# Kernel tuning notes

Measured on AMD Instinct MI355X. Metric: run time of the kernel, lower is better.

Reference implementation:

```python
import jax, jax.numpy as jnp
import numpy as np

NUM_HEADS = 8

def setup_inputs() -> dict:
    key = jax.random.key(0)
    ks = jax.random.split(key, 6)
    B, nW, F_W, ED = 8, 64, 128, 512
    x = jax.random.normal(ks[0], (B * nW, F_W, ED), dtype=jnp.float32)
    adj_mask = jax.random.normal(ks[1], (B, NUM_HEADS, F_W, F_W), dtype=jnp.float32)
    qkv_w = jax.random.normal(ks[2], (ED, 3 * ED), dtype=jnp.float32) * (ED ** -0.5)
    qkv_b = jax.random.normal(ks[3], (3 * ED,), dtype=jnp.float32) * 0.02
    proj_w = jax.random.normal(ks[4], (ED, ED), dtype=jnp.float32) * (ED ** -0.5)
    proj_b = jax.random.normal(ks[5], (ED,), dtype=jnp.float32) * 0.02
    return {"x": x, "adj_mask": adj_mask, "qkv_w": qkv_w, "qkv_b": qkv_b,
            "proj_w": proj_w, "proj_b": proj_b, "B": B, "nW": nW}

def reference(x, adj_mask, qkv_w, qkv_b, proj_w, proj_b, B, nW):
    B_nW, F_W, ED = x.shape
    H = NUM_HEADS
    hd = ED // H
    scale = hd ** -0.5
    # qkv projection: [B_nW, F_W, 3, H, hd]
    qkv = (x @ qkv_w + qkv_b).reshape(B_nW, F_W, 3, H, hd)
    qkv = jnp.transpose(qkv, (2, 0, 3, 1, 4))  # [3, B_nW, H, F_W, hd]
    q, k, v = qkv[0], qkv[1], qkv[2]
    attn = jnp.einsum('bhqd,bhkd->bhqk', q * scale, k)  # [B_nW, H, F_W, F_W]
    # additive adjacency mask, broadcast over windows
    attn = attn.reshape(B, nW, H, F_W, F_W) + adj_mask[:, None]
    attn = attn.reshape(B_nW, H, F_W, F_W)
    attn = jax.nn.softmax(attn, axis=-1)
    out = jnp.einsum('bhqk,bhkd->bhqd', attn, v)  # [B_nW, H, F_W, hd]
    out = jnp.transpose(out, (0, 2, 1, 3)).reshape(B_nW, F_W, ED)
    return out @ proj_w + proj_b
```

## Files before the change

### kernel.cpp

```cpp
#include <hip/hip_runtime.h>

typedef __bf16 bf16_t;
typedef __bf16 bf16x8 __attribute__((ext_vector_type(8)));
typedef float f32x4 __attribute__((ext_vector_type(4)));

#define MFMA16(a, b, c) __builtin_amdgcn_mfma_f32_16x16x32_bf16(a, b, c, 0, 0, 0)

#define F_W 128
#define ED 512
#define NH 8
#define HD 64
#define NTOK 65536

typedef const __attribute__((address_space(1))) void gvoid_t;
typedef __attribute__((address_space(3))) void lvoid_t;
__device__ __forceinline__ void gload16(const void* g, void* l) {
    __builtin_amdgcn_global_load_lds((gvoid_t*)g, (lvoid_t*)l, 16, 0, 0);
}

__device__ __forceinline__ int swz32(int row) { return ((row >> 1) & 3) << 3; }

__global__ __launch_bounds__(256) void prep_kernel(
    const float* __restrict__ qkv_w,
    const float* __restrict__ proj_w,
    bf16_t* __restrict__ qkv_wt,
    bf16_t* __restrict__ proj_wt) {
    int idx = blockIdx.x * 256 + threadIdx.x;
    if (idx < 1536 * 512) {
        int n = idx >> 9, k = idx & 511;
        qkv_wt[idx] = (bf16_t)qkv_w[k * 1536 + n];
    }
    if (idx < 512 * 512) {
        int n = idx >> 9, k = idx & 511;
        proj_wt[idx] = (bf16_t)proj_w[k * 512 + n];
    }
}

__global__ __launch_bounds__(256) void prep_x_kernel(
    const float* __restrict__ x, bf16_t* __restrict__ xbf) {
    size_t i = ((size_t)blockIdx.x * 256 + threadIdx.x) * 8;
    float4 v0 = *(const float4*)(x + i);
    float4 v1 = *(const float4*)(x + i + 4);
    bf16x8 o = {(bf16_t)v0.x, (bf16_t)v0.y, (bf16_t)v0.z, (bf16_t)v0.w,
                (bf16_t)v1.x, (bf16_t)v1.y, (bf16_t)v1.z, (bf16_t)v1.w};
    *(bf16x8*)(xbf + i) = o;
}

__global__ __launch_bounds__(256, 2) void qkv_gemm_kernel(
    const bf16_t* __restrict__ xbf,
    const bf16_t* __restrict__ qkv_wt,
    const float* __restrict__ qkv_b,
    bf16_t* qk_ws,
    bf16_t* vt_ws) {
    __shared__ __align__(16) char sm[49152];
    bf16_t* tb = (bf16_t*)sm;

    const int tid = threadIdx.x;
    const int wave = tid >> 6, lane = tid & 63;
    const int lrow = lane & 15, lgrp = lane >> 4;
    const int wm = wave >> 1, wn = wave & 1;
    const int bid = blockIdx.x;
    const int idx = bid >> 3;
    const int mt_l = idx / 6;
    const int nt = idx - mt_l * 6;
    const int mtile = (bid & 7) * 64 + mt_l;
    const size_t m0 = (size_t)mtile * 128;
    const int n0 = nt * 256;

    const int row16 = lane >> 2;
    const int scol = ((lane & 3) * 8) ^ swz32(row16);

    f32x4 acc[4][8];
#pragma unroll
    for (int mf = 0; mf < 4; ++mf)
#pragma unroll
        for (int nf = 0; nf < 8; ++nf) acc[mf][nf] = (f32x4)0.0f;

    for (int kc = 0; kc < 8; ++kc) {
        const int k0 = kc * 64;
        __syncthreads();
#pragma unroll
        for (int s = 0; s < 2; ++s) {
            bf16_t* As = (bf16_t*)(sm + s * 8192);
            bf16_t* Bs = (bf16_t*)(sm + 16384 + s * 16384);
#pragma unroll
            for (int i = 0; i < 2; ++i) {
                int c = wave * 2 + i;
                gload16(xbf + (m0 + c * 16 + row16) * 512 + k0 + s * 32 + scol,
                        As + c * 512);
            }
#pragma unroll
            for (int i = 0; i < 4; ++i) {
                int c = wave * 4 + i;
                gload16(qkv_wt + (size_t)(n0 + c * 16 + row16) * 512 + k0 + s * 32 + scol,
                        Bs + c * 512);
            }
        }
        __syncthreads();

#pragma unroll
        for (int kb = 0; kb < 2; ++kb) {
            bf16_t* As = (bf16_t*)(sm + kb * 8192);
            bf16_t* Bs = (bf16_t*)(sm + 16384 + kb * 16384);
            bf16x8 a[4], b[8];
#pragma unroll
            for (int mf = 0; mf < 4; ++mf) {
                int row = wm * 64 + mf * 16 + lrow;
                a[mf] = *(const bf16x8*)(As + row * 32 + ((lgrp * 8) ^ swz32(row)));
            }
#pragma unroll
            for (int nf = 0; nf < 8; ++nf) {
                int rw = wn * 128 + nf * 16 + lrow;
                b[nf] = *(const bf16x8*)(Bs + rw * 32 + ((lgrp * 8) ^ swz32(rw)));
            }
#pragma unroll
            for (int mf = 0; mf < 4; ++mf)
#pragma unroll
                for (int nf = 0; nf < 8; ++nf)
                    acc[mf][nf] = MFMA16(a[mf], b[nf], acc[mf][nf]);
        }
    }

    if (nt < 4) {
        const float scale = (nt < 2) ? 0.125f : 1.0f;
#pragma unroll
        for (int nf = 0; nf < 8; ++nf) {
            int col = n0 + wn * 128 + nf * 16 + lrow;
            float bv = qkv_b[col];
#pragma unroll
            for (int mf = 0; mf < 4; ++mf)
#pragma unroll
                for (int j = 0; j < 4; ++j) {
                    int r = wm * 64 + mf * 16 + lgrp * 4 + j;
                    qk_ws[(m0 + r) * 1024 + col] =
                        (bf16_t)((acc[mf][nf][j] + bv) * scale);
                }
        }
    } else {
#pragma unroll
        for (int hh = 0; hh < 4; ++hh) {
            int h = (nt - 4) * 4 + hh;
            __syncthreads();
            if (wn == (hh >> 1)) {
#pragma unroll
                for (int nfl = 0; nfl < 4; ++nfl) {
                    int nf = (hh & 1) * 4 + nfl;
                    int d = nfl * 16 + lrow;
                    float bv = qkv_b[1024 + (nt - 4) * 256 + hh * 64 + d];
#pragma unroll
                    for (int mf = 0; mf < 4; ++mf)
#pragma unroll
                        for (int j = 0; j < 4; ++j) {
                            int r = wm * 64 + mf * 16 + lgrp * 4 + j;
                            tb[r * 72 + d] = (bf16_t)(acc[mf][nf][j] + bv);
                        }
                }
            }
            __syncthreads();
            {
                int d = tid & 63;
                int kh = tid >> 6;
                bf16_t* outp = vt_ws + ((size_t)(mtile * 8 + h) * 64 + d) * 128 + kh * 32;
#pragma unroll
                for (int o = 0; o < 4; ++o) {
                    bf16x8 v;
#pragma unroll
                    for (int e = 0; e < 8; ++e)
                        v[e] = tb[(kh * 32 + o * 8 + e) * 72 + d];
                    *(bf16x8*)(outp + o * 8) = v;
                }
            }
        }
    }
}

__global__ __launch_bounds__(512, 4) void attn_kernel(
    bf16_t* qk_ws,
    const bf16_t* __restrict__ vt_ws,
    const float* __restrict__ adj) {
    __shared__ __align__(16) char sm[32768];
    bf16_t* k_lds  = (bf16_t*)sm;
    bf16_t* vt_lds = (bf16_t*)(sm + 16384);
    bf16_t* pbuf   = (bf16_t*)sm;

    const int tid = threadIdx.x;
    const int wave = tid >> 6, lane = tid & 63;
    const int lrow = lane & 15, lgrp = lane >> 4;
    const int bid = blockIdx.x;
    const int w = (bid & 7) * 64 + (bid >> 6);
    const int h = (bid >> 3) & 7;
    const int bidx = bid & 7;

    bf16_t* qrow = qk_ws + (size_t)w * 128 * 1024;

    {
        const int krow_l = lane >> 3;
        const int kcol_l = ((lane & 7) * 8) ^ ((krow_l & 7) << 3);
#pragma unroll
        for (int i = 0; i < 2; ++i) {
            int c = wave * 2 + i;
            gload16(qrow + (size_t)(c * 8 + krow_l) * 1024 + 512 + h * 64 + kcol_l,
                    k_lds + c * 512);
        }
    }
    {
        const bf16_t* vtb = vt_ws + (size_t)(w * 8 + h) * 64 * 128;
        const int vrow_l = lane >> 4;
#pragma unroll
        for (int i = 0; i < 2; ++i) {
            int c = wave * 2 + i;
            int d = c * 4 + vrow_l;
            int vcol = ((lane & 15) * 8) ^ ((d & 7) << 3);
            gload16(vtb + (size_t)d * 128 + vcol, vt_lds + c * 512);
        }
    }
    bf16x8 aq[2];
    {
        int row = wave * 16 + lrow;
#pragma unroll
        for (int kb = 0; kb < 2; ++kb)
            aq[kb] = *(const bf16x8*)(qrow + (size_t)row * 1024 + h * 64 + kb * 32 + lgrp * 8);
    }
    __syncthreads();

    f32x4 sacc[8];
#pragma unroll
    for (int nf = 0; nf < 8; ++nf) sacc[nf] = (f32x4)0.0f;
#pragma unroll
    for (int kb = 0; kb < 2; ++kb) {
        bf16x8 b[8];
#pragma unroll
        for (int nf = 0; nf < 8; ++nf) {
            int row = nf * 16 + lrow;
            b[nf] = *(const bf16x8*)(k_lds + row * 64 + ((kb * 32 + lgrp * 8) ^ ((row & 7) << 3)));
        }
#pragma unroll
        for (int nf = 0; nf < 8; ++nf)
            sacc[nf] = MFMA16(aq[kb], b[nf], sacc[nf]);
    }

    const float* mbase = adj + ((size_t)(bidx * NH + h)) * F_W * F_W;
#pragma unroll
    for (int j = 0; j < 4; ++j) {
        int row = wave * 16 + lgrp * 4 + j;
        const float* mrow = mbase + (size_t)row * F_W;
        float mx = -1e30f;
#pragma unroll
        for (int nf = 0; nf < 8; ++nf) {
            sacc[nf][j] += mrow[nf * 16 + lrow];
            mx = fmaxf(mx, sacc[nf][j]);
        }
#pragma unroll
        for (int d = 1; d < 16; d <<= 1) mx = fmaxf(mx, __shfl_xor(mx, d));
        float sum = 0.f;
#pragma unroll
        for (int nf = 0; nf < 8; ++nf) {
            float p = exp2f((sacc[nf][j] - mx) * 1.44269504f);
            sacc[nf][j] = p;
            sum += p;
        }
#pragma unroll
        for (int d = 1; d < 16; d <<= 1) sum += __shfl_xor(sum, d);
        float r = 1.0f / sum;
#pragma unroll
        for (int nf = 0; nf < 8; ++nf) sacc[nf][j] *= r;
    }
    __syncthreads();

    f32x4 oacc[4];
#pragma unroll
    for (int nf = 0; nf < 4; ++nf) oacc[nf] = (f32x4)0.0f;

#pragma unroll
    for (int kb = 0; kb < 4; ++kb) {
#pragma unroll
        for (int nn = 0; nn < 2; ++nn) {
            int nf = kb * 2 + nn;
            int kk = nn * 16 + lrow;
#pragma unroll
            for (int j = 0; j < 4; ++j) {
                int r = wave * 16 + lgrp * 4 + j;
                pbuf[r * 40 + kk] = (bf16_t)(sacc[nf][j]);
            }
        }
        __syncthreads();
        bf16x8 a = *(const bf16x8*)(pbuf + (wave * 16 + lrow) * 40 + lgrp * 8);
        bf16x8 b[4];
#pragma unroll
        for (int nf = 0; nf < 4; ++nf) {
            int d = nf * 16 + lrow;
            b[nf] = *(const bf16x8*)(vt_lds + d * 128 + ((kb * 32 + lgrp * 8) ^ ((d & 7) << 3)));
        }
#pragma unroll
        for (int nf = 0; nf < 4; ++nf)
            oacc[nf] = MFMA16(a, b[nf], oacc[nf]);
        __syncthreads();
    }

#pragma unroll
    for (int nf = 0; nf < 4; ++nf) {
        int ocol = h * 64 + nf * 16 + lrow;
#pragma unroll
        for (int j = 0; j < 4; ++j) {
            int r = wave * 16 + lgrp * 4 + j;
            qrow[(size_t)r * 1024 + ocol] = (bf16_t)oacc[nf][j];
        }
    }
}

__global__ __launch_bounds__(256, 2) void proj_kernel(
    const bf16_t* __restrict__ a_g,
    const bf16_t* __restrict__ bt_g,
    const float* __restrict__ bias,
    float* __restrict__ out) {
    __shared__ __align__(16) char sm_[49152];
    const int tid = threadIdx.x;
    const int wave = tid >> 6, lane = tid & 63;
    const int lrow = lane & 15, lgrp = lane >> 4;
    const int wm = wave >> 1, wn = wave & 1;
    const int bid = blockIdx.x;
    const int idx = bid >> 3;
    const int mtile = (bid & 7) * 64 + (idx >> 1);
    const int ntile = idx & 1;
    const size_t m0 = (size_t)mtile * 128;
    const int n0 = ntile * 256;
    const int row16 = lane >> 2;
    const int scol = ((lane & 3) * 8) ^ swz32(row16);

    f32x4 acc[4][8];
#pragma unroll
    for (int mf = 0; mf < 4; ++mf)
#pragma unroll
        for (int nf = 0; nf < 8; ++nf) acc[mf][nf] = (f32x4)0.0f;

    for (int kc = 0; kc < 8; ++kc) {
        const int k0 = kc * 64;
        __syncthreads();
#pragma unroll
        for (int s = 0; s < 2; ++s) {
            bf16_t* As = (bf16_t*)(sm_ + s * 8192);
            bf16_t* Bs = (bf16_t*)(sm_ + 16384 + s * 16384);
#pragma unroll
            for (int i = 0; i < 2; ++i) {
                int c = wave * 2 + i;
                gload16(a_g + (m0 + c * 16 + row16) * 1024 + k0 + s * 32 + scol,
                        As + c * 512);
            }
#pragma unroll
            for (int i = 0; i < 4; ++i) {
                int c = wave * 4 + i;
                gload16(bt_g + (size_t)(n0 + c * 16 + row16) * 512 + k0 + s * 32 + scol,
                        Bs + c * 512);
            }
        }
        __syncthreads();

#pragma unroll
        for (int kb = 0; kb < 2; ++kb) {
            bf16_t* As = (bf16_t*)(sm_ + kb * 8192);
            bf16_t* Bs = (bf16_t*)(sm_ + 16384 + kb * 16384);
            bf16x8 a[4], b[8];
#pragma unroll
            for (int mf = 0; mf < 4; ++mf) {
                int row = wm * 64 + mf * 16 + lrow;
                a[mf] = *(const bf16x8*)(As + row * 32 + ((lgrp * 8) ^ swz32(row)));
            }
#pragma unroll
            for (int nf = 0; nf < 8; ++nf) {
                int rw = wn * 128 + nf * 16 + lrow;
                b[nf] = *(const bf16x8*)(Bs + rw * 32 + ((lgrp * 8) ^ swz32(rw)));
            }
#pragma unroll
            for (int mf = 0; mf < 4; ++mf)
#pragma unroll
                for (int nf = 0; nf < 8; ++nf)
                    acc[mf][nf] = MFMA16(a[mf], b[nf], acc[mf][nf]);
        }
    }

#pragma unroll
    for (int nf = 0; nf < 8; ++nf) {
        int col = n0 + wn * 128 + nf * 16 + lrow;
        float bv = bias[col];
#pragma unroll
        for (int mf = 0; mf < 4; ++mf)
#pragma unroll
            for (int j = 0; j < 4; ++j) {
                size_t row = m0 + wm * 64 + mf * 16 + lgrp * 4 + j;
                out[row * 512 + col] = acc[mf][nf][j] + bv;
            }
    }
}

extern "C" void kernel_launch(void* const* d_in, const int* in_sizes, int n_in,
                              void* d_out, int out_size, void* d_ws, size_t ws_size,
                              hipStream_t stream) {
    const float* x      = (const float*)d_in[0];
    const float* adj    = (const float*)d_in[1];
    const float* qkv_w  = (const float*)d_in[2];
    const float* qkv_b  = (const float*)d_in[3];
    const float* proj_w = (const float*)d_in[4];
    const float* proj_b = (const float*)d_in[5];
    float* out = (float*)d_out;

    bf16_t* qk_ws   = (bf16_t*)d_ws;
    bf16_t* vt_ws   = qk_ws + (size_t)NTOK * 1024;
    bf16_t* qkv_wt  = vt_ws + (size_t)4096 * 64 * 128;
    bf16_t* proj_wt = qkv_wt + 1536 * 512;
    bf16_t* xbf = (bf16_t*)d_out;

    prep_kernel<<<3072, 256, 0, stream>>>(qkv_w, proj_w, qkv_wt, proj_wt);
    prep_x_kernel<<<NTOK * ED / 8 / 256, 256, 0, stream>>>(x, xbf);
    qkv_gemm_kernel<<<3072, 256, 0, stream>>>(xbf, qkv_wt, qkv_b, qk_ws, vt_ws);
    attn_kernel<<<4096, 512, 0, stream>>>(qk_ws, vt_ws, adj);
    proj_kernel<<<1024, 256, 0, stream>>>(qk_ws, proj_wt, proj_b, out);
}
```

Before: 299.8 us.

## Enlarge QKV GEMM tile to 256x256 with a 4-stage LDS pipeline

The QKV projection GEMM now runs 512 threads per block on a 256x256 output tile instead of 256 threads on a 128x256 tile. It keeps a four-deep ring of LDS buffers (128KB) filled by direct global-to-LDS loads, using explicit vmcnt waits, barriers and raised scheduling priority around the MFMA blocks. The aim is to overlap global loads with matrix math and to reuse each loaded operand across more output. The V-transpose epilogue is adjusted so one tile covers two windows. The large LDS footprint limits each CU to one block, and the hand-tuned wait counts are fragile.

```diff
diff --git a/kernel.cpp b/kernel.cpp
--- a/kernel.cpp
+++ b/kernel.cpp
@@ -46,92 +46,140 @@
     *(bf16x8*)(xbf + i) = o;
 }
 
-__global__ __launch_bounds__(256, 2) void qkv_gemm_kernel(
+__global__ __launch_bounds__(512, 2) void qkv_gemm_kernel(
     const bf16_t* __restrict__ xbf,
     const bf16_t* __restrict__ qkv_wt,
     const float* __restrict__ qkv_b,
     bf16_t* qk_ws,
     bf16_t* vt_ws) {
-    __shared__ __align__(16) char sm[49152];
-    bf16_t* tb = (bf16_t*)sm;
+    __shared__ __align__(16) char smem[131072];
+    bf16_t* tb = (bf16_t*)smem;
 
     const int tid = threadIdx.x;
     const int wave = tid >> 6, lane = tid & 63;
     const int lrow = lane & 15, lgrp = lane >> 4;
-    const int wm = wave >> 1, wn = wave & 1;
+    const int wm = wave >> 2;
+    const int wn = wave & 3;
     const int bid = blockIdx.x;
     const int idx = bid >> 3;
     const int mt_l = idx / 6;
     const int nt = idx - mt_l * 6;
-    const int mtile = (bid & 7) * 64 + mt_l;
-    const size_t m0 = (size_t)mtile * 128;
+    const int mtile = (bid & 7) * 32 + mt_l;
+    const size_t m0 = (size_t)mtile * 256;
     const int n0 = nt * 256;
 
     const int row16 = lane >> 2;
     const int scol = ((lane & 3) * 8) ^ swz32(row16);
 
-    f32x4 acc[4][8];
-#pragma unroll
-    for (int mf = 0; mf < 4; ++mf)
-#pragma unroll
-        for (int nf = 0; nf < 8; ++nf) acc[mf][nf] = (f32x4)0.0f;
-
-    for (int kc = 0; kc < 8; ++kc) {
-        const int k0 = kc * 64;
-        __syncthreads();
-#pragma unroll
-        for (int s = 0; s < 2; ++s) {
-            bf16_t* As = (bf16_t*)(sm + s * 8192);
-            bf16_t* Bs = (bf16_t*)(sm + 16384 + s * 16384);
-#pragma unroll
-            for (int i = 0; i < 2; ++i) {
-                int c = wave * 2 + i;
-                gload16(xbf + (m0 + c * 16 + row16) * 512 + k0 + s * 32 + scol,
-                        As + c * 512);
-            }
-#pragma unroll
-            for (int i = 0; i < 4; ++i) {
-                int c = wave * 4 + i;
-                gload16(qkv_wt + (size_t)(n0 + c * 16 + row16) * 512 + k0 + s * 32 + scol,
-                        Bs + c * 512);
-            }
-        }
-        __syncthreads();
-
-#pragma unroll
-        for (int kb = 0; kb < 2; ++kb) {
-            bf16_t* As = (bf16_t*)(sm + kb * 8192);
-            bf16_t* Bs = (bf16_t*)(sm + 16384 + kb * 16384);
-            bf16x8 a[4], b[8];
-#pragma unroll
-            for (int mf = 0; mf < 4; ++mf) {
-                int row = wm * 64 + mf * 16 + lrow;
-                a[mf] = *(const bf16x8*)(As + row * 32 + ((lgrp * 8) ^ swz32(row)));
-            }
-#pragma unroll
-            for (int nf = 0; nf < 8; ++nf) {
-                int rw = wn * 128 + nf * 16 + lrow;
-                b[nf] = *(const bf16x8*)(Bs + rw * 32 + ((lgrp * 8) ^ swz32(rw)));
-            }
-#pragma unroll
-            for (int mf = 0; mf < 4; ++mf)
-#pragma unroll
-                for (int nf = 0; nf < 8; ++nf)
-                    acc[mf][nf] = MFMA16(a[mf], b[nf], acc[mf][nf]);
-        }
-    }
+    f32x4 acc[8][4];
+#pragma unroll
+    for (int mf = 0; mf < 8; ++mf)
+#pragma unroll
+        for (int nf = 0; nf < 4; ++nf) acc[mf][nf] = (f32x4)0.0f;
+
+    auto stageA = [&](int g) {
+        bf16_t* As = (bf16_t*)(smem + (g & 3) * 32768);
+        const int k0 = g * 32;
+#pragma unroll
+        for (int i = 0; i < 2; ++i) {
+            int c = wave * 2 + i;
+            gload16(xbf + (m0 + c * 16 + row16) * 512 + k0 + scol, As + c * 512);
+        }
+    };
+    auto stageB = [&](int g) {
+        bf16_t* Bs = (bf16_t*)(smem + (g & 3) * 32768 + 16384);
+        const int k0 = g * 32;
+#pragma unroll
+        for (int i = 0; i < 2; ++i) {
+            int c = wave * 2 + i;
+            gload16(qkv_wt + (size_t)(n0 + c * 16 + row16) * 512 + k0 + scol,
+                    Bs + c * 512);
+        }
+    };
+
+    auto khalf = [&](int h) {
+        bf16_t* As = (bf16_t*)(smem + (h & 3) * 32768);
+        bf16_t* Bs = (bf16_t*)(smem + (h & 3) * 32768 + 16384);
+        bf16x8 a[4], b[4];
+#pragma unroll
+        for (int i = 0; i < 4; ++i) {
+            int row = wm * 128 + i * 16 + lrow;
+            a[i] = *(const bf16x8*)(As + row * 32 + ((lgrp * 8) ^ swz32(row)));
+        }
+#pragma unroll
+        for (int i = 0; i < 4; ++i) {
+            int rw = wn * 64 + i * 16 + lrow;
+            b[i] = *(const bf16x8*)(Bs + rw * 32 + ((lgrp * 8) ^ swz32(rw)));
+        }
+        if (h + 3 < 16) stageA(h + 3);
+        __builtin_amdgcn_sched_barrier(0);
+        __builtin_amdgcn_s_barrier();
+        asm volatile("s_waitcnt lgkmcnt(0)" ::: "memory");
+        __builtin_amdgcn_sched_barrier(0);
+        __builtin_amdgcn_s_setprio(1);
+#pragma unroll
+        for (int i = 0; i < 4; ++i)
+#pragma unroll
+            for (int nf = 0; nf < 4; ++nf)
+                acc[i][nf] = MFMA16(a[i], b[nf], acc[i][nf]);
+        __builtin_amdgcn_s_setprio(0);
+        __builtin_amdgcn_sched_barrier(0);
+        __builtin_amdgcn_s_barrier();
+#pragma unroll
+        for (int i = 0; i < 4; ++i) {
+            int row = wm * 128 + (4 + i) * 16 + lrow;
+            a[i] = *(const bf16x8*)(As + row * 32 + ((lgrp * 8) ^ swz32(row)));
+        }
+        if (h + 3 < 16) stageB(h + 3);
+        __builtin_amdgcn_sched_barrier(0);
+        __builtin_amdgcn_s_barrier();
+        asm volatile("s_waitcnt lgkmcnt(0)" ::: "memory");
+        __builtin_amdgcn_sched_barrier(0);
+        __builtin_amdgcn_s_setprio(1);
+#pragma unroll
+        for (int i = 0; i < 4; ++i)
+#pragma unroll
+            for (int nf = 0; nf < 4; ++nf)
+                acc[4 + i][nf] = MFMA16(a[i], b[nf], acc[4 + i][nf]);
+        __builtin_amdgcn_s_setprio(0);
+        __builtin_amdgcn_sched_barrier(0);
+    };
+
+    stageA(0); stageB(0);
+    stageA(1); stageB(1);
+    stageA(2); stageB(2);
+    asm volatile("s_waitcnt vmcnt(8)" ::: "memory");
+    __builtin_amdgcn_sched_barrier(0);
+    __builtin_amdgcn_s_barrier();
+
+    for (int h = 0; h < 13; ++h) {
+        khalf(h);
+        asm volatile("s_waitcnt vmcnt(8)" ::: "memory");
+        __builtin_amdgcn_sched_barrier(0);
+        __builtin_amdgcn_s_barrier();
+    }
+    khalf(13);
+    asm volatile("s_waitcnt vmcnt(4)" ::: "memory");
+    __builtin_amdgcn_sched_barrier(0);
+    __builtin_amdgcn_s_barrier();
+    khalf(14);
+    asm volatile("s_waitcnt vmcnt(0)" ::: "memory");
+    __builtin_amdgcn_sched_barrier(0);
+    __builtin_amdgcn_s_barrier();
+    khalf(15);
+    __builtin_amdgcn_s_barrier();
 
     if (nt < 4) {
         const float scale = (nt < 2) ? 0.125f : 1.0f;
 #pragma unroll
-        for (int nf = 0; nf < 8; ++nf) {
-            int col = n0 + wn * 128 + nf * 16 + lrow;
+        for (int nf = 0; nf < 4; ++nf) {
+            int col = n0 + wn * 64 + nf * 16 + lrow;
             float bv = qkv_b[col];
 #pragma unroll
-            for (int mf = 0; mf < 4; ++mf)
+            for (int mf = 0; mf < 8; ++mf)
 #pragma unroll
                 for (int j = 0; j < 4; ++j) {
-                    int r = wm * 64 + mf * 16 + lgrp * 4 + j;
+                    int r = wm * 128 + mf * 16 + lgrp * 4 + j;
                     qk_ws[(m0 + r) * 1024 + col] =
                         (bf16_t)((acc[mf][nf][j] + bv) * scale);
                 }
@@ -141,17 +189,16 @@
         for (int hh = 0; hh < 4; ++hh) {
             int h = (nt - 4) * 4 + hh;
             __syncthreads();
-            if (wn == (hh >> 1)) {
-#pragma unroll
-                for (int nfl = 0; nfl < 4; ++nfl) {
-                    int nf = (hh & 1) * 4 + nfl;
-                    int d = nfl * 16 + lrow;
+            if (wn == hh) {
+#pragma unroll
+                for (int nf = 0; nf < 4; ++nf) {
+                    int d = nf * 16 + lrow;
                     float bv = qkv_b[1024 + (nt - 4) * 256 + hh * 64 + d];
 #pragma unroll
-                    for (int mf = 0; mf < 4; ++mf)
+                    for (int mf = 0; mf < 8; ++mf)
 #pragma unroll
                         for (int j = 0; j < 4; ++j) {
-                            int r = wm * 64 + mf * 16 + lgrp * 4 + j;
+                            int r = wm * 128 + mf * 16 + lgrp * 4 + j;
                             tb[r * 72 + d] = (bf16_t)(acc[mf][nf][j] + bv);
                         }
                 }
@@ -160,14 +207,16 @@
             {
                 int d = tid & 63;
                 int kh = tid >> 6;
-                bf16_t* outp = vt_ws + ((size_t)(mtile * 8 + h) * 64 + d) * 128 + kh * 32;
 #pragma unroll
                 for (int o = 0; o < 4; ++o) {
+                    int k = kh * 32 + o * 8;
+                    int win = mtile * 2 + (k >> 7);
                     bf16x8 v;
 #pragma unroll
                     for (int e = 0; e < 8; ++e)
-                        v[e] = tb[(kh * 32 + o * 8 + e) * 72 + d];
-                    *(bf16x8*)(outp + o * 8) = v;
+                        v[e] = tb[(k + e) * 72 + d];
+                    *(bf16x8*)(vt_ws + ((size_t)(win * 8 + h) * 64 + d) * 128 +
+                               (k & 127)) = v;
                 }
             }
         }
@@ -411,7 +460,7 @@
 
     prep_kernel<<<3072, 256, 0, stream>>>(qkv_w, proj_w, qkv_wt, proj_wt);
     prep_x_kernel<<<NTOK * ED / 8 / 256, 256, 0, stream>>>(x, xbf);
-    qkv_gemm_kernel<<<3072, 256, 0, stream>>>(xbf, qkv_wt, qkv_b, qk_ws, vt_ws);
+    qkv_gemm_kernel<<<1536, 512, 0, stream>>>(xbf, qkv_wt, qkv_b, qk_ws, vt_ws);
     attn_kernel<<<4096, 512, 0, stream>>>(qk_ws, vt_ws, adj);
     proj_kernel<<<1024, 256, 0, stream>>>(qk_ws, proj_wt, proj_b, out);
 }
```

Result: slower. 309.6 us (+3.3%).
